# Kernel tuning notes

Hardware: AMD Instinct MI355X
Metric: run time of the kernel (lower is better)

Reference implementation:

```python
import jax, jax.numpy as jnp
import numpy as np

B, T, C = 4, 2048, 1024
H = 16
D = C // H  # head_size = 64


def setup_inputs() -> dict:
    key = jax.random.key(0)
    ks = jax.random.split(key, 9)
    s = 1.0 / np.sqrt(C).astype(np.float32)
    return {
        "x": jax.random.normal(ks[0], (B, T, C), dtype=jnp.float32),
        "Wq": jax.random.normal(ks[1], (C, C), dtype=jnp.float32) * s,
        "bq": jnp.zeros((C,), dtype=jnp.float32),
        "Wk": jax.random.normal(ks[2], (C, C), dtype=jnp.float32) * s,
        "bk": jnp.zeros((C,), dtype=jnp.float32),
        "Wv": jax.random.normal(ks[3], (C, C), dtype=jnp.float32) * s,
        "bv": jnp.zeros((C,), dtype=jnp.float32),
        "Wp": jax.random.normal(ks[4], (C, C), dtype=jnp.float32) * s,
        "bp": jnp.zeros((C,), dtype=jnp.float32),
    }


def reference(x, Wq, bq, Wk, bk, Wv, bv, Wp, bp):
    # Linear projections, then split heads: (B, T, C) -> (B, H, T, D)
    def heads(t):
        return t.reshape(B, T, H, D).transpose(0, 2, 1, 3)

    q = heads(x @ Wq + bq)
    k = heads(x @ Wk + bk)
    v = heads(x @ Wv + bv)

    scale = 1.0 / np.sqrt(D).astype(np.float32)
    att = jnp.einsum("bhqd,bhkd->bhqk", q, k) * scale  # (B, H, T, T)
    att = jax.nn.softmax(att, axis=-1)
    y = jnp.einsum("bhqk,bhkd->bhqd", att, v)  # (B, H, T, D)
    y = y.transpose(0, 2, 1, 3).reshape(B, T, C)
    return y @ Wp + bp
```

## Files before the change

### kernel.cpp

```cpp
#include <hip/hip_runtime.h>

typedef unsigned int uint;
typedef unsigned short ushort;

typedef __bf16 bf16x8 __attribute__((ext_vector_type(8)));
typedef __bf16 bf16x2 __attribute__((ext_vector_type(2)));
typedef float f32x4 __attribute__((ext_vector_type(4)));
typedef float f32x16 __attribute__((ext_vector_type(16)));
typedef uint uint2v __attribute__((ext_vector_type(2)));

union U4 { uint4 u; bf16x8 v; };
union UB2 { bf16x2 v; uint u; };

__device__ __forceinline__ ushort f2bf(float f){
  uint u = __float_as_uint(f);
  u += 0x7fffu + ((u >> 16) & 1u);
  return (ushort)(u >> 16);
}

__device__ __forceinline__ uint packbf(float lo, float hi){
  UB2 t; t.v[0] = (__bf16)lo; t.v[1] = (__bf16)hi;
  return t.u;
}

__device__ __forceinline__ float exp2a(float x){
  float r; asm("v_exp_f32 %0, %1" : "=v"(r) : "v"(x)); return r;
}

__device__ __forceinline__ void gload16(const void* g, void* l){
  __builtin_amdgcn_global_load_lds((const __attribute__((address_space(1))) uint*)g,
                                   (__attribute__((address_space(3))) uint*)l, 16, 0, 0);
}

__device__ __forceinline__ f32x16 mfma32(U4 a, U4 b, f32x16 c){
  return __builtin_amdgcn_mfma_f32_32x32x16_bf16(a.v, b.v, c, 0, 0, 0);
}

__global__ __launch_bounds__(256, 2) void gemm_bt(
    const ushort* __restrict__ Ahp, const ushort* __restrict__ Bhp,
    const float* __restrict__ bias, void* __restrict__ outp,
    int mode, float oscale)
{
  __shared__ uint4 smem4[2048];
  char* sAh = (char*)smem4;
  char* sBh = (char*)smem4 + 16384;

  const int tid  = threadIdx.x;
  const int lane = tid & 63;
  const int wid  = tid >> 6;
  const int wm = (wid >> 1) * 64;
  const int wn = (wid & 1) * 64;

  int lin = blockIdx.y * 64 + blockIdx.x;
  int xcd = lin & 7, j = lin >> 3;
  const long tm = (long)(xcd * 8 + (j & 7)) * 128;
  const long tn = (long)(j >> 3) * 128;

  const char* gA = (const char*)Ahp;
  const char* gB = (const char*)Bhp;

  f32x4 acc[4][4] = {};

  for (int ks = 0; ks < 16; ks++){
    const int koff = ks * 128;
    #pragma unroll
    for (int c = 0; c < 4; c++){
      int o   = (tid + 256*c) * 16;
      int row = o >> 7;
      int src = (o & 127) ^ ((row & 7) << 4);
      gload16(gA + (tm + row)*2048 + koff + src, sAh + o);
      gload16(gB + (tn + row)*2048 + koff + src, sBh + o);
    }
    __syncthreads();
    #pragma unroll
    for (int k = 0; k < 2; k++){
      const int kb = k*64 + (lane >> 4)*16;
      U4 ah[4], bh[4];
      #pragma unroll
      for (int m = 0; m < 4; m++){
        int row = wm + m*16 + (lane & 15);
        ah[m].u = *(const uint4*)(sAh + row*128 + (kb ^ ((row & 7) << 4)));
      }
      #pragma unroll
      for (int n = 0; n < 4; n++){
        int row = wn + n*16 + (lane & 15);
        bh[n].u = *(const uint4*)(sBh + row*128 + (kb ^ ((row & 7) << 4)));
      }
      __builtin_amdgcn_s_setprio(1);
      #pragma unroll
      for (int m = 0; m < 4; m++)
      #pragma unroll
      for (int n = 0; n < 4; n++)
        acc[m][n] = __builtin_amdgcn_mfma_f32_16x16x32_bf16(ah[m].v, bh[n].v, acc[m][n], 0,0,0);
      __builtin_amdgcn_s_setprio(0);
    }
    __syncthreads();
  }

  #pragma unroll
  for (int n = 0; n < 4; n++){
    int colg = (int)tn + wn + n*16 + (lane & 15);
    float bv = bias[colg];
    #pragma unroll
    for (int m = 0; m < 4; m++){
      int rowg0 = (int)tm + wm + m*16 + ((lane >> 4) * 4);
      float v0 = (acc[m][n][0] + bv) * oscale;
      float v1 = (acc[m][n][1] + bv) * oscale;
      float v2 = (acc[m][n][2] + bv) * oscale;
      float v3 = (acc[m][n][3] + bv) * oscale;
      if (mode == 0){
        ushort* o = (ushort*)outp;
        o[(long)(rowg0+0)*1024 + colg] = f2bf(v0);
        o[(long)(rowg0+1)*1024 + colg] = f2bf(v1);
        o[(long)(rowg0+2)*1024 + colg] = f2bf(v2);
        o[(long)(rowg0+3)*1024 + colg] = f2bf(v3);
      } else if (mode == 1){
        int b = rowg0 >> 11, t0 = rowg0 & 2047;
        int h = colg >> 6, d = colg & 63;
        ushort4 o4;
        o4.x = f2bf(v0); o4.y = f2bf(v1); o4.z = f2bf(v2); o4.w = f2bf(v3);
        *(ushort4*)&((ushort*)outp)[(((long)(b*16 + h))*64 + d)*2048 + t0] = o4;
      } else {
        float* o = (float*)outp;
        o[(long)(rowg0+0)*1024 + colg] = v0;
        o[(long)(rowg0+1)*1024 + colg] = v1;
        o[(long)(rowg0+2)*1024 + colg] = v2;
        o[(long)(rowg0+3)*1024 + colg] = v3;
      }
    }
  }
}

__device__ __forceinline__ void mkfrag(const uint (&pk)[8], U4 (&out)[2])
{
  #pragma unroll
  for (int kl = 0; kl < 2; kl++){
    int bb = kl*4;
    uint2v r02 = __builtin_amdgcn_permlane32_swap(pk[bb+0], pk[bb+2], false, false);
    uint2v r13 = __builtin_amdgcn_permlane32_swap(pk[bb+1], pk[bb+3], false, false);
    out[kl].u = make_uint4(r02[0], r13[0], r02[1], r13[1]);
  }
}

__global__ __launch_bounds__(256, 2) void attn_kernel(
    const ushort* __restrict__ Qg, const ushort* __restrict__ Kg,
    const ushort* __restrict__ Vtg, ushort* __restrict__ Yg)
{
  __shared__ uint4 smem[2048];
  char* sK0 = (char*)smem;
  char* sV0 = (char*)smem + 8192;
  char* sK1 = (char*)smem + 16384;
  char* sV1 = (char*)smem + 24576;

  const int tid  = threadIdx.x;
  const int lane = tid & 63;
  const int w    = tid >> 6;
  const int ql   = lane & 31;
  const int hh   = lane >> 5;

  int lin = blockIdx.y * 8 + blockIdx.x;
  int xcd = lin & 7, jj = lin >> 3;
  const int bh  = (jj >> 3) * 8 + xcd;
  const int qb  = jj & 7;
  const int tq0 = qb * 256 + w * 64;
  const int b = bh >> 4, h = bh & 15;

  U4 qf[2][4];
  #pragma unroll
  for (int g = 0; g < 2; g++){
    const char* qrow = (const char*)Qg + (long)(b*2048 + tq0 + g*32 + ql)*2048 + h*128 + hh*16;
    #pragma unroll
    for (int c = 0; c < 4; c++) qf[g][c].u = *(const uint4*)(qrow + c*32);
  }

  f32x16 y00 = {}, y01 = {}, y10 = {}, y11 = {};
  float ls0 = 0.f, ls1 = 0.f;

  const char* kbase = (const char*)Kg  + (long)b*2048*2048 + h*128;
  const char* vbase = (const char*)Vtg + (long)bh*64*4096;

  auto stage = [&](char* dK, char* dV, int kc){
    #pragma unroll
    for (int c2 = 0; c2 < 2; c2++){
      int o   = tid*16 + c2*4096;
      int row = o >> 7;
      int src = (o & 127) ^ ((row & 7) << 4);
      gload16(kbase + (long)(kc*64 + row)*2048 + src, dK + o);
      gload16(vbase + (long)row*4096 + (long)kc*128 + src, dV + o);
    }
  };

  auto sm = [&](f32x16& s, float& ls, uint (&pk)[8]){
    float ps = 0.f;
    #pragma unroll
    for (int r = 0; r < 16; r++){ s[r] = exp2a(s[r]); ps += s[r]; }
    ls += ps;
    #pragma unroll
    for (int i = 0; i < 8; i++) pk[i] = packbf(s[2*i], s[2*i+1]);
  };

  auto body = [&](int kc, char* cK, char* cV, char* nK, char* nV){
    if (kc < 31){
      stage(nK, nV, kc + 1);
      asm volatile("s_waitcnt vmcnt(4)" ::: "memory");
    } else {
      asm volatile("s_waitcnt vmcnt(0)" ::: "memory");
    }
    __builtin_amdgcn_s_barrier();

    f32x16 s00 = {}, s10 = {};
    __builtin_amdgcn_s_setprio(1);
    #pragma unroll
    for (int ksd = 0; ksd < 4; ksd++){
      int kb = ksd*32 + hh*16;
      int r = ql;
      U4 a; a.u = *(const uint4*)(cK + r*128 + (kb ^ ((r & 7) << 4)));
      s00 = mfma32(a, qf[0][ksd], s00);
      s10 = mfma32(a, qf[1][ksd], s10);
    }
    __builtin_amdgcn_s_setprio(0);

    uint pk00[8], pk10[8];
    sm(s00, ls0, pk00); sm(s10, ls1, pk10);
    U4 f0[2], f1[2];
    mkfrag(pk00, f0); mkfrag(pk10, f1);

    f32x16 s01 = {}, s11 = {};
    __builtin_amdgcn_s_setprio(1);
    #pragma unroll
    for (int ksd = 0; ksd < 4; ksd++){
      int kb = ksd*32 + hh*16;
      int r = 32 + ql;
      U4 a; a.u = *(const uint4*)(cK + r*128 + (kb ^ ((r & 7) << 4)));
      s01 = mfma32(a, qf[0][ksd], s01);
      s11 = mfma32(a, qf[1][ksd], s11);
    }

    #pragma unroll
    for (int kl = 0; kl < 2; kl++){
      int kvo = kl*32 + hh*16;
      U4 a0, a1;
      { int r = ql;      a0.u = *(const uint4*)(cV + r*128 + (kvo ^ ((r & 7) << 4))); }
      { int r = 32 + ql; a1.u = *(const uint4*)(cV + r*128 + (kvo ^ ((r & 7) << 4))); }
      y00 = mfma32(a0, f0[kl], y00);
      y01 = mfma32(a1, f0[kl], y01);
      y10 = mfma32(a0, f1[kl], y10);
      y11 = mfma32(a1, f1[kl], y11);
    }
    __builtin_amdgcn_s_setprio(0);

    uint pk01[8], pk11[8];
    sm(s01, ls0, pk01); sm(s11, ls1, pk11);
    mkfrag(pk01, f0); mkfrag(pk11, f1);

    __builtin_amdgcn_s_setprio(1);
    #pragma unroll
    for (int kl = 0; kl < 2; kl++){
      int kvo = 64 + kl*32 + hh*16;
      U4 a0, a1;
      { int r = ql;      a0.u = *(const uint4*)(cV + r*128 + (kvo ^ ((r & 7) << 4))); }
      { int r = 32 + ql; a1.u = *(const uint4*)(cV + r*128 + (kvo ^ ((r & 7) << 4))); }
      y00 = mfma32(a0, f0[kl], y00);
      y01 = mfma32(a1, f0[kl], y01);
      y10 = mfma32(a0, f1[kl], y10);
      y11 = mfma32(a1, f1[kl], y11);
    }
    __builtin_amdgcn_s_setprio(0);

    if (kc < 31){
      asm volatile("" ::: "memory");
      __builtin_amdgcn_s_barrier();
    }
  };

  stage(sK0, sV0, 0);
  for (int kc2 = 0; kc2 < 16; kc2++){
    body(2*kc2 + 0, sK0, sV0, sK1, sV1);
    body(2*kc2 + 1, sK1, sV1, sK0, sV0);
  }

  #pragma unroll
  for (int g = 0; g < 2; g++){
    f32x16& t0 = g ? y10 : y00;
    f32x16& t1 = g ? y11 : y01;
    float ls   = g ? ls1 : ls0;
    float lt   = ls + __shfl_xor(ls, 32);
    float inv  = 1.0f / lt;
    int tq = tq0 + g*32 + ql;
    ushort* yrow = Yg + ((long)b*2048 + tq)*1024 + h*64;
    #pragma unroll
    for (int qi = 0; qi < 4; qi++){
      ushort4 o0, o1;
      o0.x = f2bf(t0[qi*4+0]*inv); o0.y = f2bf(t0[qi*4+1]*inv);
      o0.z = f2bf(t0[qi*4+2]*inv); o0.w = f2bf(t0[qi*4+3]*inv);
      o1.x = f2bf(t1[qi*4+0]*inv); o1.y = f2bf(t1[qi*4+1]*inv);
      o1.z = f2bf(t1[qi*4+2]*inv); o1.w = f2bf(t1[qi*4+3]*inv);
      *(ushort4*)(yrow + qi*8 + hh*4)      = o0;
      *(ushort4*)(yrow + 32 + qi*8 + hh*4) = o1;
    }
  }
}

__global__ void cast_x_kernel(const float* __restrict__ x, ushort* __restrict__ xh)
{
  int i = blockIdx.x*256 + threadIdx.x;
  float4 v = ((const float4*)x)[i];
  ushort4 h;
  h.x = f2bf(v.x); h.y = f2bf(v.y); h.z = f2bf(v.z); h.w = f2bf(v.w);
  ((ushort4*)xh)[i] = h;
}

__global__ void wsplit_kernel(const float* __restrict__ W, ushort* __restrict__ Th)
{
  __shared__ float tile[64][65];
  const int tid = threadIdx.x;
  const int k0 = blockIdx.x * 64;
  const int n0 = blockIdx.y * 64;
  #pragma unroll
  for (int c = 0; c < 4; c++){
    int idx = tid + 256*c;
    int r = idx >> 4, c4 = idx & 15;
    float4 v = *(const float4*)&W[(long)(k0 + r)*1024 + n0 + c4*4];
    tile[r][c4*4+0] = v.x; tile[r][c4*4+1] = v.y;
    tile[r][c4*4+2] = v.z; tile[r][c4*4+3] = v.w;
  }
  __syncthreads();
  #pragma unroll
  for (int c = 0; c < 4; c++){
    int idx = tid + 256*c;
    int nr = idx >> 4, k4 = idx & 15;
    ushort4 hh;
    hh.x = f2bf(tile[k4*4+0][nr]); hh.y = f2bf(tile[k4*4+1][nr]);
    hh.z = f2bf(tile[k4*4+2][nr]); hh.w = f2bf(tile[k4*4+3][nr]);
    *(ushort4*)&Th[(long)(n0 + nr)*1024 + k0 + k4*4] = hh;
  }
}

extern "C" void kernel_launch(void* const* d_in, const int* in_sizes, int n_in,
                              void* d_out, int out_size, void* d_ws, size_t ws_size,
                              hipStream_t stream)
{
  const float* x  = (const float*)d_in[0];
  const float* Wq = (const float*)d_in[1];
  const float* bq = (const float*)d_in[2];
  const float* Wk = (const float*)d_in[3];
  const float* bk = (const float*)d_in[4];
  const float* Wv = (const float*)d_in[5];
  const float* bv = (const float*)d_in[6];
  const float* Wp = (const float*)d_in[7];
  const float* bp = (const float*)d_in[8];

  char* ws = (char*)d_ws;
  const size_t SZ_X = 16777216;
  const size_t SZ_W = 2097152;
  ushort* xh  = (ushort*)(ws);
  ushort* wqh = (ushort*)(ws + SZ_X);
  ushort* wkh = (ushort*)(ws + SZ_X + 1*SZ_W);
  ushort* wvh = (ushort*)(ws + SZ_X + 2*SZ_W);
  ushort* wph = (ushort*)(ws + SZ_X + 3*SZ_W);
  ushort* Qb  = (ushort*)(ws + SZ_X + 4*SZ_W);
  ushort* Kb  = (ushort*)(ws + 2*SZ_X + 4*SZ_W);
  ushort* Vtb = (ushort*)(ws + 3*SZ_X + 4*SZ_W);
  ushort* Yb  = (ushort*)(ws + 4*SZ_X + 4*SZ_W);

  cast_x_kernel<<<8192, 256, 0, stream>>>(x, xh);
  dim3 wg(16, 16);
  wsplit_kernel<<<wg, 256, 0, stream>>>(Wq, wqh);
  wsplit_kernel<<<wg, 256, 0, stream>>>(Wk, wkh);
  wsplit_kernel<<<wg, 256, 0, stream>>>(Wv, wvh);
  wsplit_kernel<<<wg, 256, 0, stream>>>(Wp, wph);

  dim3 gg(64, 8);
  gemm_bt<<<gg, 256, 0, stream>>>(xh, wqh, bq, Qb, 0, 0.18033688f);
  gemm_bt<<<gg, 256, 0, stream>>>(xh, wkh, bk, Kb, 0, 1.0f);
  gemm_bt<<<gg, 256, 0, stream>>>(xh, wvh, bv, Vtb, 1, 1.0f);

  dim3 ag(8, 64);
  attn_kernel<<<ag, 256, 0, stream>>>(Qb, Kb, Vtb, Yb);

  gemm_bt<<<gg, 256, 0, stream>>>(Yb, wph, bp, d_out, 2, 1.0f);
}
```

Measured before the change: 288.8 us.

## Merge QKV GEMMs and weight casts into single launches, shrink attention blocks

Merges the three Q/K/V projection GEMMs into one launch over a 64x24 grid, choosing weights, bias and output layout per block. The four weight-cast launches become one with a z dimension. The output GEMM gets its own specialised kernel, and the attention kernel drops to 128 threads per block with twice as many blocks, each thread doing more staging loads. The goal is fewer launches, a fuller GPU in the QKV stage, and better attention occupancy and balance, at the cost of branching on w and an occupancy hint of 3 on the QKV kernel that may not be reachable.

```diff
diff --git a/kernel.cpp b/kernel.cpp
--- a/kernel.cpp
+++ b/kernel.cpp
@@ -36,10 +36,12 @@
   return __builtin_amdgcn_mfma_f32_32x32x16_bf16(a.v, b.v, c, 0, 0, 0);
 }
 
-__global__ __launch_bounds__(256, 2) void gemm_bt(
-    const ushort* __restrict__ Ahp, const ushort* __restrict__ Bhp,
-    const float* __restrict__ bias, void* __restrict__ outp,
-    int mode, float oscale)
+__global__ __launch_bounds__(256, 3) void gemm_qkv(
+    const ushort* __restrict__ xh, const ushort* __restrict__ wbase,
+    const float* __restrict__ bq, const float* __restrict__ bk,
+    const float* __restrict__ bv,
+    ushort* __restrict__ Qb, ushort* __restrict__ Kb, ushort* __restrict__ Vtb,
+    float qscale)
 {
   __shared__ uint4 smem4[2048];
   char* sAh = (char*)smem4;
@@ -51,17 +53,21 @@
   const int wm = (wid >> 1) * 64;
   const int wn = (wid & 1) * 64;
 
-  int lin = blockIdx.y * 64 + blockIdx.x;
-  int xcd = lin & 7, j = lin >> 3;
-  const long tm = (long)(xcd * 8 + (j & 7)) * 128;
-  const long tn = (long)(j >> 3) * 128;
-
-  const char* gA = (const char*)Ahp;
-  const char* gB = (const char*)Bhp;
+  int hwlin = blockIdx.y * 64 + blockIdx.x;
+  int xcd = hwlin & 7, io = hwlin >> 3;
+  int mb  = xcd * 8 + (io & 7);
+  int nv  = io >> 3;
+  int nb  = nv & 7;
+  int w   = nv >> 3;
+  const long tm = (long)mb * 128;
+  const long tn = (long)nb * 128;
+
+  const char* gA = (const char*)xh;
+  const char* gB = (const char*)(wbase + (long)w * 1048576);
 
   f32x4 acc[4][4] = {};
 
-  for (int ks = 0; ks < 16; ks++){
+  for (int ks = 0; ks < 8; ks++){
     const int koff = ks * 128;
     #pragma unroll
     for (int c = 0; c < 4; c++){
@@ -96,37 +102,143 @@
     }
     __syncthreads();
   }
+  for (int ks = 8; ks < 16; ks++){
+    const int koff = ks * 128;
+    #pragma unroll
+    for (int c = 0; c < 4; c++){
+      int o   = (tid + 256*c) * 16;
+      int row = o >> 7;
+      int src = (o & 127) ^ ((row & 7) << 4);
+      gload16(gA + (tm + row)*2048 + koff + src, sAh + o);
+      gload16(gB + (tn + row)*2048 + koff + src, sBh + o);
+    }
+    __syncthreads();
+    #pragma unroll
+    for (int k = 0; k < 2; k++){
+      const int kb = k*64 + (lane >> 4)*16;
+      U4 ah[4], bh[4];
+      #pragma unroll
+      for (int m = 0; m < 4; m++){
+        int row = wm + m*16 + (lane & 15);
+        ah[m].u = *(const uint4*)(sAh + row*128 + (kb ^ ((row & 7) << 4)));
+      }
+      #pragma unroll
+      for (int n = 0; n < 4; n++){
+        int row = wn + n*16 + (lane & 15);
+        bh[n].u = *(const uint4*)(sBh + row*128 + (kb ^ ((row & 7) << 4)));
+      }
+      __builtin_amdgcn_s_setprio(1);
+      #pragma unroll
+      for (int m = 0; m < 4; m++)
+      #pragma unroll
+      for (int n = 0; n < 4; n++)
+        acc[m][n] = __builtin_amdgcn_mfma_f32_16x16x32_bf16(ah[m].v, bh[n].v, acc[m][n], 0,0,0);
+      __builtin_amdgcn_s_setprio(0);
+    }
+    __syncthreads();
+  }
+
+  const float* bias = (w == 0) ? bq : (w == 1) ? bk : bv;
+  const float oscale = (w == 0) ? qscale : 1.0f;
 
   #pragma unroll
   for (int n = 0; n < 4; n++){
     int colg = (int)tn + wn + n*16 + (lane & 15);
-    float bv = bias[colg];
+    float bv_ = bias[colg];
     #pragma unroll
     for (int m = 0; m < 4; m++){
       int rowg0 = (int)tm + wm + m*16 + ((lane >> 4) * 4);
-      float v0 = (acc[m][n][0] + bv) * oscale;
-      float v1 = (acc[m][n][1] + bv) * oscale;
-      float v2 = (acc[m][n][2] + bv) * oscale;
-      float v3 = (acc[m][n][3] + bv) * oscale;
-      if (mode == 0){
-        ushort* o = (ushort*)outp;
+      float v0 = (acc[m][n][0] + bv_) * oscale;
+      float v1 = (acc[m][n][1] + bv_) * oscale;
+      float v2 = (acc[m][n][2] + bv_) * oscale;
+      float v3 = (acc[m][n][3] + bv_) * oscale;
+      if (w < 2){
+        ushort* o = (w == 0) ? Qb : Kb;
         o[(long)(rowg0+0)*1024 + colg] = f2bf(v0);
         o[(long)(rowg0+1)*1024 + colg] = f2bf(v1);
         o[(long)(rowg0+2)*1024 + colg] = f2bf(v2);
         o[(long)(rowg0+3)*1024 + colg] = f2bf(v3);
-      } else if (mode == 1){
+      } else {
         int b = rowg0 >> 11, t0 = rowg0 & 2047;
         int h = colg >> 6, d = colg & 63;
         ushort4 o4;
         o4.x = f2bf(v0); o4.y = f2bf(v1); o4.z = f2bf(v2); o4.w = f2bf(v3);
-        *(ushort4*)&((ushort*)outp)[(((long)(b*16 + h))*64 + d)*2048 + t0] = o4;
-      } else {
-        float* o = (float*)outp;
-        o[(long)(rowg0+0)*1024 + colg] = v0;
-        o[(long)(rowg0+1)*1024 + colg] = v1;
-        o[(long)(rowg0+2)*1024 + colg] = v2;
-        o[(long)(rowg0+3)*1024 + colg] = v3;
-      }
+        *(ushort4*)&Vtb[(((long)(b*16 + h))*64 + d)*2048 + t0] = o4;
+      }
+    }
+  }
+}
+
+__global__ __launch_bounds__(256, 2) void gemm_out(
+    const ushort* __restrict__ Ahp, const ushort* __restrict__ Bhp,
+    const float* __restrict__ bias, float* __restrict__ outp)
+{
+  __shared__ uint4 smem4[2048];
+  char* sAh = (char*)smem4;
+  char* sBh = (char*)smem4 + 16384;
+
+  const int tid  = threadIdx.x;
+  const int lane = tid & 63;
+  const int wid  = tid >> 6;
+  const int wm = (wid >> 1) * 64;
+  const int wn = (wid & 1) * 64;
+
+  int lin = blockIdx.y * 64 + blockIdx.x;
+  int xcd = lin & 7, j = lin >> 3;
+  const long tm = (long)(xcd * 8 + (j & 7)) * 128;
+  const long tn = (long)(j >> 3) * 128;
+
+  const char* gA = (const char*)Ahp;
+  const char* gB = (const char*)Bhp;
+
+  f32x4 acc[4][4] = {};
+
+  for (int ks = 0; ks < 16; ks++){
+    const int koff = ks * 128;
+    #pragma unroll
+    for (int c = 0; c < 4; c++){
+      int o   = (tid + 256*c) * 16;
+      int row = o >> 7;
+      int src = (o & 127) ^ ((row & 7) << 4);
+      gload16(gA + (tm + row)*2048 + koff + src, sAh + o);
+      gload16(gB + (tn + row)*2048 + koff + src, sBh + o);
+    }
+    __syncthreads();
+    #pragma unroll
+    for (int k = 0; k < 2; k++){
+      const int kb = k*64 + (lane >> 4)*16;
+      U4 ah[4], bh[4];
+      #pragma unroll
+      for (int m = 0; m < 4; m++){
+        int row = wm + m*16 + (lane & 15);
+        ah[m].u = *(const uint4*)(sAh + row*128 + (kb ^ ((row & 7) << 4)));
+      }
+      #pragma unroll
+      for (int n = 0; n < 4; n++){
+        int row = wn + n*16 + (lane & 15);
+        bh[n].u = *(const uint4*)(sBh + row*128 + (kb ^ ((row & 7) << 4)));
+      }
+      __builtin_amdgcn_s_setprio(1);
+      #pragma unroll
+      for (int m = 0; m < 4; m++)
+      #pragma unroll
+      for (int n = 0; n < 4; n++)
+        acc[m][n] = __builtin_amdgcn_mfma_f32_16x16x32_bf16(ah[m].v, bh[n].v, acc[m][n], 0,0,0);
+      __builtin_amdgcn_s_setprio(0);
+    }
+    __syncthreads();
+  }
+
+  #pragma unroll
+  for (int n = 0; n < 4; n++){
+    int colg = (int)tn + wn + n*16 + (lane & 15);
+    float bv_ = bias[colg];
+    #pragma unroll
+    for (int m = 0; m < 4; m++){
+      int rowg0 = (int)tm + wm + m*16 + ((lane >> 4) * 4);
+      #pragma unroll
+      for (int r = 0; r < 4; r++)
+        outp[(long)(rowg0+r)*1024 + colg] = acc[m][n][r] + bv_;
     }
   }
 }
@@ -142,7 +254,7 @@
   }
 }
 
-__global__ __launch_bounds__(256, 2) void attn_kernel(
+__global__ __launch_bounds__(128, 2) void attn_kernel(
     const ushort* __restrict__ Qg, const ushort* __restrict__ Kg,
     const ushort* __restrict__ Vtg, ushort* __restrict__ Yg)
 {
@@ -158,11 +270,11 @@
   const int ql   = lane & 31;
   const int hh   = lane >> 5;
 
-  int lin = blockIdx.y * 8 + blockIdx.x;
-  int xcd = lin & 7, jj = lin >> 3;
-  const int bh  = (jj >> 3) * 8 + xcd;
-  const int qb  = jj & 7;
-  const int tq0 = qb * 256 + w * 64;
+  int lin = blockIdx.y * 16 + blockIdx.x;
+  int xcd = lin & 7, j = lin >> 3;
+  const int bh  = (j >> 4) * 8 + xcd;
+  const int qb  = j & 15;
+  const int tq0 = qb * 128 + w * 64;
   const int b = bh >> 4, h = bh & 15;
 
   U4 qf[2][4];
@@ -181,8 +293,8 @@
 
   auto stage = [&](char* dK, char* dV, int kc){
     #pragma unroll
-    for (int c2 = 0; c2 < 2; c2++){
-      int o   = tid*16 + c2*4096;
+    for (int c2 = 0; c2 < 4; c2++){
+      int o   = tid*16 + c2*2048;
       int row = o >> 7;
       int src = (o & 127) ^ ((row & 7) << 4);
       gload16(kbase + (long)(kc*64 + row)*2048 + src, dK + o);
@@ -202,7 +314,7 @@
   auto body = [&](int kc, char* cK, char* cV, char* nK, char* nV){
     if (kc < 31){
       stage(nK, nV, kc + 1);
-      asm volatile("s_waitcnt vmcnt(4)" ::: "memory");
+      asm volatile("s_waitcnt vmcnt(8)" ::: "memory");
     } else {
       asm volatile("s_waitcnt vmcnt(0)" ::: "memory");
     }
@@ -310,9 +422,14 @@
   ((ushort4*)xh)[i] = h;
 }
 
-__global__ void wsplit_kernel(const float* __restrict__ W, ushort* __restrict__ Th)
+__global__ void wsplit_kernel(const float* __restrict__ W0, const float* __restrict__ W1,
+                              const float* __restrict__ W2, const float* __restrict__ W3,
+                              ushort* __restrict__ outbase)
 {
   __shared__ float tile[64][65];
+  const int z = blockIdx.z;
+  const float* W = (z == 0) ? W0 : (z == 1) ? W1 : (z == 2) ? W2 : W3;
+  ushort* Th = outbase + (long)z * 1048576;
   const int tid = threadIdx.x;
   const int k0 = blockIdx.x * 64;
   const int n0 = blockIdx.y * 64;
@@ -355,8 +472,6 @@
   const size_t SZ_W = 2097152;
   ushort* xh  = (ushort*)(ws);
   ushort* wqh = (ushort*)(ws + SZ_X);
-  ushort* wkh = (ushort*)(ws + SZ_X + 1*SZ_W);
-  ushort* wvh = (ushort*)(ws + SZ_X + 2*SZ_W);
   ushort* wph = (ushort*)(ws + SZ_X + 3*SZ_W);
   ushort* Qb  = (ushort*)(ws + SZ_X + 4*SZ_W);
   ushort* Kb  = (ushort*)(ws + 2*SZ_X + 4*SZ_W);
@@ -364,19 +479,12 @@
   ushort* Yb  = (ushort*)(ws + 4*SZ_X + 4*SZ_W);
 
   cast_x_kernel<<<8192, 256, 0, stream>>>(x, xh);
-  dim3 wg(16, 16);
-  wsplit_kernel<<<wg, 256, 0, stream>>>(Wq, wqh);
-  wsplit_kernel<<<wg, 256, 0, stream>>>(Wk, wkh);
-  wsplit_kernel<<<wg, 256, 0, stream>>>(Wv, wvh);
-  wsplit_kernel<<<wg, 256, 0, stream>>>(Wp, wph);
-
-  dim3 gg(64, 8);
-  gemm_bt<<<gg, 256, 0, stream>>>(xh, wqh, bq, Qb, 0, 0.18033688f);
-  gemm_bt<<<gg, 256, 0, stream>>>(xh, wkh, bk, Kb, 0, 1.0f);
-  gemm_bt<<<gg, 256, 0, stream>>>(xh, wvh, bv, Vtb, 1, 1.0f);
-
-  dim3 ag(8, 64);
-  attn_kernel<<<ag, 256, 0, stream>>>(Qb, Kb, Vtb, Yb);
-
-  gemm_bt<<<gg, 256, 0, stream>>>(Yb, wph, bp, d_out, 2, 1.0f);
-}
+  wsplit_kernel<<<dim3(16,16,4), 256, 0, stream>>>(Wq, Wk, Wv, Wp, wqh);
+
+  gemm_qkv<<<dim3(64,24), 256, 0, stream>>>(xh, wqh, bq, bk, bv,
+                                            Qb, Kb, Vtb, 0.18033688f);
+
+  attn_kernel<<<dim3(16,64), 128, 0, stream>>>(Qb, Kb, Vtb, Yb);
+
+  gemm_out<<<dim3(64,8), 256, 0, stream>>>(Yb, wph, bp, (float*)d_out);
+}
```

Result: faster. 272.6 us (-5.6%).
